# Kernel tuning notes

Hardware: AMD Instinct MI355X
Metric: run time of the kernel (lower is better)

The kernel has to match this reference:

```python
import jax, jax.numpy as jnp
import numpy as np

N_HOURLY = 24
D_MODEL = 512
D_POOL = D_MODEL // 4  # 128


def setup_inputs() -> dict:
    key = jax.random.key(0)
    ks = jax.random.split(key, 9)
    B, E, D = 64, 2048, D_MODEL
    day_embed = jax.random.normal(ks[0], (B, D), dtype=jnp.float32)
    episode_ctx = jax.random.normal(ks[1], (B, E, D), dtype=jnp.float32)
    n_episodes = jax.random.randint(ks[2], (B,), 0, E)
    d_in = D + N_HOURLY * D_POOL  # 3584
    W_pool = jax.random.normal(ks[3], (D, D_POOL), dtype=jnp.float32) * (1.0 / np.sqrt(D))
    b_pool = jnp.zeros((D_POOL,), dtype=jnp.float32)
    W1 = jax.random.normal(ks[4], (d_in, D), dtype=jnp.float32) * (1.0 / np.sqrt(d_in))
    b1 = jnp.zeros((D,), dtype=jnp.float32)
    W2 = jax.random.normal(ks[5], (D, 2), dtype=jnp.float32) * (1.0 / np.sqrt(D))
    b2 = jnp.zeros((2,), dtype=jnp.float32)
    return {"day_embed": day_embed, "episode_ctx": episode_ctx, "n_episodes": n_episodes,
            "W_pool": W_pool, "b_pool": b_pool, "W1": W1, "b1": b1, "W2": W2, "b2": b2}


def reference(day_embed, episode_ctx, n_episodes, W_pool, b_pool, W1, b1, W2, b2):
    B, E, D = episode_ctx.shape
    # project all (padded) episodes: [B, E, D/4]
    feats = jnp.einsum('bed,dk->bek', episode_ctx, W_pool) + b_pool
    # bin_size = max(n_ep // 24, 1); episode j (j < n_ep) belongs to bin j // bin_size,
    # dropped if bin >= 24. This exactly reproduces the torch slicing loop.
    bs = jnp.maximum(n_episodes // N_HOURLY, 1)  # [B]
    j = jnp.arange(E)
    bin_id = j[None, :] // bs[:, None]                       # [B, E]
    valid = (j[None, :] < n_episodes[:, None]) & (bin_id < N_HOURLY)
    hmask = (bin_id[:, None, :] == jnp.arange(N_HOURLY)[None, :, None]) & valid[:, None, :]
    mf = hmask.astype(feats.dtype)                           # [B, H, E]
    sums = jnp.einsum('bhe,bek->bhk', mf, feats)             # [B, H, D/4]
    counts = mf.sum(-1)                                      # [B, H]
    hourly = jnp.where(counts[..., None] > 0,
                       sums / jnp.maximum(counts, 1.0)[..., None],
                       jnp.zeros_like(sums))
    x = jnp.concatenate([day_embed, hourly.reshape(B, -1)], axis=-1)  # [B, 3584]
    h = jax.nn.gelu(x @ W1 + b1, approximate=False)  # torch nn.GELU default = exact erf
    return h @ W2 + b2  # [B, 2]; dropout is identity in eval mode
```

## Files before the change

kernel.cpp:

```cpp
#include <hip/hip_runtime.h>
#include <math.h>

#define NH    24
#define DM    512
#define DP    128
#define EMAX  2048
#define DIN   3584
#define B     64


__global__ void binpool_kernel(const float* __restrict__ day_embed,
                               const float* __restrict__ episode_ctx,
                               const int* __restrict__ n_episodes,
                               const float* __restrict__ W_pool,
                               const float* __restrict__ b_pool,
                               float* __restrict__ x_T) {
    const int h = blockIdx.x;
    const int b = blockIdx.y;
    const int t = threadIdx.x;

    if (h == NH) {
        for (int i = t; i < DM; i += 256)
            x_T[(size_t)i * B + b] = day_embed[b * DM + i];
        return;
    }

    const int n  = n_episodes[b];
    int bs = n / NH; if (bs < 1) bs = 1;
    const int lo = h * bs;
    int hi = lo + bs; if (hi > n) hi = n;
    int count = hi - lo; if (count < 0) count = 0;

    __shared__ float sh_mean[DM];

    float a0 = 0.f, a1 = 0.f;
    const float2* base = (const float2*)episode_ctx
                       + (size_t)b * EMAX * (DM / 2) + t;
    #pragma unroll 4
    for (int e = lo; e < hi; ++e) {
        float2 v = base[(size_t)e * (DM / 2)];
        a0 += v.x;
        a1 += v.y;
    }
    const float inv = (count > 0) ? (1.0f / (float)count) : 0.0f;
    sh_mean[2 * t]     = a0 * inv;
    sh_mean[2 * t + 1] = a1 * inv;
    __syncthreads();

    if (t < 64) {
        float c0 = 0.f, c1 = 0.f;
        const float2* wp = (const float2*)W_pool + t;
        #pragma unroll 4
        for (int d = 0; d < DM; ++d) {
            float m = sh_mean[d];
            float2 w = wp[(size_t)d * (DP / 2)];
            c0 += m * w.x;
            c1 += m * w.y;
        }
        const int row = DM + h * DP + 2 * t;
        if (count > 0) {
            x_T[(size_t)row * B + b]       = c0 + b_pool[2 * t];
            x_T[(size_t)(row + 1) * B + b] = c1 + b_pool[2 * t + 1];
        } else {
            x_T[(size_t)row * B + b]       = 0.f;
            x_T[(size_t)(row + 1) * B + b] = 0.f;
        }
    }
}

__global__ void mlp1_kernel(const float* __restrict__ x_T,
                            const float* __restrict__ W1,
                            float* __restrict__ part) {
    const int c = blockIdx.x;
    const int s = blockIdx.y;
    const int t = threadIdx.x;
    const int w = t >> 6;
    const int lane = t & 63;

    float acc[16];
    #pragma unroll
    for (int j = 0; j < 16; ++j) acc[j] = 0.f;

    const int k0 = 448 * s + 112 * w;
    const float* wbase = W1 + (size_t)k0 * DM + 16 * c;
    const float* xbase = x_T + (size_t)k0 * B + lane;

    #pragma unroll 4
    for (int ki = 0; ki < 112; ++ki) {
        float xv = xbase[ki * B];
        const float* wrow = wbase + (size_t)ki * DM;
        #pragma unroll
        for (int j = 0; j < 16; ++j)
            acc[j] += xv * wrow[j];
    }

    __shared__ float red[4][64][17];
    #pragma unroll
    for (int j = 0; j < 16; ++j)
        red[w][lane][j] = acc[j];
    __syncthreads();

    for (int idx = t; idx < 1024; idx += 256) {
        const int row = idx >> 4;
        const int j   = idx & 15;
        float v = red[0][row][j] + red[1][row][j] + red[2][row][j] + red[3][row][j];
        part[(size_t)s * (B * DM) + (size_t)row * DM + 16 * c + j] = v;
    }
}

__global__ void epilogue_kernel(const float* __restrict__ part,
                                const float* __restrict__ b1,
                                float* __restrict__ hbuf) {
    const int idx = blockIdx.x * 256 + threadIdx.x;
    const int col = idx & (DM - 1);
    float v = 0.f;
    #pragma unroll
    for (int s = 0; s < 8; ++s)
        v += part[(size_t)s * (B * DM) + idx];
    v += b1[col];
    v = 0.5f * v * (1.0f + erff(v * 0.70710678118654752f));
    hbuf[idx] = v;
}

__global__ void mlp2_kernel(const float* __restrict__ hbuf,
                            const float* __restrict__ W2,
                            const float* __restrict__ b2,
                            float* __restrict__ out) {
    const int b = blockIdx.x;
    const int t = threadIdx.x;
    float a0 = 0.f, a1 = 0.f;
    #pragma unroll
    for (int i = t; i < DM; i += 64) {
        float hv = hbuf[(size_t)b * DM + i];
        float2 w = ((const float2*)W2)[i];
        a0 += hv * w.x;
        a1 += hv * w.y;
    }
    #pragma unroll
    for (int off = 32; off > 0; off >>= 1) {
        a0 += __shfl_down(a0, off);
        a1 += __shfl_down(a1, off);
    }
    if (t == 0) {
        out[b * 2]     = a0 + b2[0];
        out[b * 2 + 1] = a1 + b2[1];
    }
}

extern "C" void kernel_launch(void* const* d_in, const int* in_sizes, int n_in,
                              void* d_out, int out_size, void* d_ws, size_t ws_size,
                              hipStream_t stream) {
    const float* day_embed   = (const float*)d_in[0];
    const float* episode_ctx = (const float*)d_in[1];
    const int*   n_episodes  = (const int*)d_in[2];
    const float* W_pool      = (const float*)d_in[3];
    const float* b_pool      = (const float*)d_in[4];
    const float* W1          = (const float*)d_in[5];
    const float* b1          = (const float*)d_in[6];
    const float* W2          = (const float*)d_in[7];
    const float* b2          = (const float*)d_in[8];
    float* out = (float*)d_out;

    float* x_T  = (float*)d_ws;
    float* part = x_T + (size_t)DIN * B;
    float* hbuf = part + (size_t)8 * B * DM;

    dim3 gA(NH + 1, B);
    binpool_kernel<<<gA, 256, 0, stream>>>(day_embed, episode_ctx, n_episodes,
                                           W_pool, b_pool, x_T);
    dim3 gB(32, 8);
    mlp1_kernel<<<gB, 256, 0, stream>>>(x_T, W1, part);

    epilogue_kernel<<<128, 256, 0, stream>>>(part, b1, hbuf);

    mlp2_kernel<<<64, 64, 0, stream>>>(hbuf, W2, b2, out);
}
```

Before: 427.3 us.

## Vectorize binpool and mlp1 loads, fuse epilogue and mlp2 into tail kernel

```diff
diff --git a/kernel.cpp b/kernel.cpp
--- a/kernel.cpp
+++ b/kernel.cpp
@@ -31,20 +31,31 @@
     int hi = lo + bs; if (hi > n) hi = n;
     int count = hi - lo; if (count < 0) count = 0;
 
-    __shared__ float sh_mean[DM];
+    __shared__ float4 sh4[256];
+    __shared__ float  sh_mean[DM];
 
-    float a0 = 0.f, a1 = 0.f;
-    const float2* base = (const float2*)episode_ctx
-                       + (size_t)b * EMAX * (DM / 2) + t;
-    #pragma unroll 4
-    for (int e = lo; e < hi; ++e) {
-        float2 v = base[(size_t)e * (DM / 2)];
-        a0 += v.x;
-        a1 += v.y;
+    const int p  = t & 127;
+    const int eo = t >> 7;
+
+    float4 a = make_float4(0.f, 0.f, 0.f, 0.f);
+    const float4* base = (const float4*)episode_ctx
+                       + (size_t)b * EMAX * (DM / 4) + p;
+    #pragma unroll 2
+    for (int e = lo + eo; e < hi; e += 2) {
+        float4 v = base[(size_t)e * (DM / 4)];
+        a.x += v.x; a.y += v.y; a.z += v.z; a.w += v.w;
     }
-    const float inv = (count > 0) ? (1.0f / (float)count) : 0.0f;
-    sh_mean[2 * t]     = a0 * inv;
-    sh_mean[2 * t + 1] = a1 * inv;
+    sh4[t] = a;
+    __syncthreads();
+
+    if (t < 128) {
+        const float inv = (count > 0) ? (1.0f / (float)count) : 0.0f;
+        float4 u = sh4[t], v = sh4[t + 128];
+        sh_mean[4 * t]     = (u.x + v.x) * inv;
+        sh_mean[4 * t + 1] = (u.y + v.y) * inv;
+        sh_mean[4 * t + 2] = (u.z + v.z) * inv;
+        sh_mean[4 * t + 3] = (u.w + v.w) * inv;
+    }
     __syncthreads();
 
     if (t < 64) {
@@ -82,16 +93,21 @@
     for (int j = 0; j < 16; ++j) acc[j] = 0.f;
 
     const int k0 = 448 * s + 112 * w;
-    const float* wbase = W1 + (size_t)k0 * DM + 16 * c;
+    const float4* wbase = (const float4*)(W1 + (size_t)k0 * DM + 16 * c);
     const float* xbase = x_T + (size_t)k0 * B + lane;
 
     #pragma unroll 4
     for (int ki = 0; ki < 112; ++ki) {
         float xv = xbase[ki * B];
-        const float* wrow = wbase + (size_t)ki * DM;
+        const float4* wrow = wbase + (size_t)ki * (DM / 4);
         #pragma unroll
-        for (int j = 0; j < 16; ++j)
-            acc[j] += xv * wrow[j];
+        for (int q = 0; q < 4; ++q) {
+            float4 wv = wrow[q];
+            acc[4 * q]     += xv * wv.x;
+            acc[4 * q + 1] += xv * wv.y;
+            acc[4 * q + 2] += xv * wv.z;
+            acc[4 * q + 3] += xv * wv.w;
+        }
     }
 
     __shared__ float red[4][64][17];
@@ -108,42 +124,46 @@
     }
 }
 
-__global__ void epilogue_kernel(const float* __restrict__ part,
-                                const float* __restrict__ b1,
-                                float* __restrict__ hbuf) {
-    const int idx = blockIdx.x * 256 + threadIdx.x;
-    const int col = idx & (DM - 1);
-    float v = 0.f;
-    #pragma unroll
-    for (int s = 0; s < 8; ++s)
-        v += part[(size_t)s * (B * DM) + idx];
-    v += b1[col];
-    v = 0.5f * v * (1.0f + erff(v * 0.70710678118654752f));
-    hbuf[idx] = v;
-}
-
-__global__ void mlp2_kernel(const float* __restrict__ hbuf,
+__global__ void tail_kernel(const float* __restrict__ part,
+                            const float* __restrict__ b1,
                             const float* __restrict__ W2,
                             const float* __restrict__ b2,
                             float* __restrict__ out) {
     const int b = blockIdx.x;
     const int t = threadIdx.x;
-    float a0 = 0.f, a1 = 0.f;
+
+    __shared__ float sh_h[DM];
+
     #pragma unroll
-    for (int i = t; i < DM; i += 64) {
-        float hv = hbuf[(size_t)b * DM + i];
-        float2 w = ((const float2*)W2)[i];
-        a0 += hv * w.x;
-        a1 += hv * w.y;
+    for (int rep = 0; rep < 2; ++rep) {
+        const int col = t + rep * 256;
+        float v = 0.f;
+        #pragma unroll
+        for (int s = 0; s < 8; ++s)
+            v += part[(size_t)s * (B * DM) + (size_t)b * DM + col];
+        v += b1[col];
+        sh_h[col] = 0.5f * v * (1.0f + erff(v * 0.70710678118654752f));
     }
-    #pragma unroll
-    for (int off = 32; off > 0; off >>= 1) {
-        a0 += __shfl_down(a0, off);
-        a1 += __shfl_down(a1, off);
-    }
-    if (t == 0) {
-        out[b * 2]     = a0 + b2[0];
-        out[b * 2 + 1] = a1 + b2[1];
+    __syncthreads();
+
+    if (t < 64) {
+        float a0 = 0.f, a1 = 0.f;
+        #pragma unroll
+        for (int i = t; i < DM; i += 64) {
+            float hv = sh_h[i];
+            float2 w = ((const float2*)W2)[i];
+            a0 += hv * w.x;
+            a1 += hv * w.y;
+        }
+        #pragma unroll
+        for (int off = 32; off > 0; off >>= 1) {
+            a0 += __shfl_down(a0, off);
+            a1 += __shfl_down(a1, off);
+        }
+        if (t == 0) {
+            out[b * 2]     = a0 + b2[0];
+            out[b * 2 + 1] = a1 + b2[1];
+        }
     }
 }
 
@@ -163,7 +183,6 @@
 
     float* x_T  = (float*)d_ws;
     float* part = x_T + (size_t)DIN * B;
-    float* hbuf = part + (size_t)8 * B * DM;
 
     dim3 gA(NH + 1, B);
     binpool_kernel<<<gA, 256, 0, stream>>>(day_embed, episode_ctx, n_episodes,
@@ -171,7 +190,5 @@
     dim3 gB(32, 8);
     mlp1_kernel<<<gB, 256, 0, stream>>>(x_T, W1, part);
 
-    epilogue_kernel<<<128, 256, 0, stream>>>(part, b1, hbuf);
-
-    mlp2_kernel<<<64, 64, 0, stream>>>(hbuf, W2, b2, out);
+    tail_kernel<<<64, 256, 0, stream>>>(part, b1, W2, b2, out);
 }
```

New measurement: 424.0 us. About the same (-0.8%).
